# Performance work log

Hardware: AMD Instinct MI355X
Metric: run time of the kernel (lower is better)

The kernel has to match this reference:

```python
import jax, jax.numpy as jnp
import numpy as np

B, S, D, H, R, P = 4, 8192, 512, 8, 64, 4
HD = D // H  # 64
EPS = 1e-6


def _sketch_p4(z, G1, G2):
    # sketchwithnegativity(z, 2): M1 = M2 = z
    inv_sqrt_r = 1.0 / np.sqrt(R).astype(np.float32)
    half = inv_sqrt_r * ((z @ G1) * (z @ G2))  # [B,H,S,R]
    return half * half  # sketch(): half * half for p=4


def setup_inputs() -> dict:
    key = jax.random.key(0)
    ks = jax.random.split(key, 16)
    lin = lambda k: jax.random.normal(k, (D, D), jnp.float32) * (1.0 / np.sqrt(D))
    g = lambda k: jax.random.normal(k, (HD, R), jnp.float32) * (1.0 / np.sqrt(R))
    return {
        "x": jax.random.normal(ks[0], (B, S, D), jnp.float32),
        "Wq": lin(ks[1]), "bq": jnp.zeros((D,), jnp.float32),
        "Wk": lin(ks[2]), "bk": jnp.zeros((D,), jnp.float32),
        "Wv": lin(ks[3]), "bv": jnp.zeros((D,), jnp.float32),
        "Wp": lin(ks[4]), "bp": jnp.zeros((D,), jnp.float32),
        "gamma_q": jnp.ones((1,), jnp.float32), "beta_q": jnp.zeros((1,), jnp.float32),
        "gamma_k": jnp.ones((1,), jnp.float32), "beta_k": jnp.zeros((1,), jnp.float32),
        "qG1": g(ks[5]), "qG2": g(ks[6]),
        "kG1": g(ks[7]), "kG2": g(ks[8]),
    }


def reference(x, Wq, bq, Wk, bk, Wv, bv, Wp, bp,
              gamma_q, beta_q, gamma_k, beta_k, qG1, qG2, kG1, kG2):
    b, s, d = x.shape
    split = lambda t: t.reshape(b, s, H, HD).transpose(0, 2, 1, 3)  # [B,H,S,HD]
    q = split(x @ Wq + bq)
    k = split(x @ Wk + bk)
    v = split(x @ Wv + bv)
    q = gamma_q * q + beta_q
    k = gamma_k * k + beta_k
    phi_q = _sketch_p4(q, qG1, qG2)  # [B,H,S,R]
    phi_k = _sketch_p4(k, kG1, kG2)  # [B,H,S,R]
    # linear-attention form of attn = (phi_q phi_k^T) / rowsum; avoids [S,S]
    kv = jnp.einsum('bhsr,bhsd->bhrd', phi_k, v)          # [B,H,R,HD]
    ksum = phi_k.sum(axis=2)                              # [B,H,R]
    num = jnp.einsum('bhqr,bhrd->bhqd', phi_q, kv)        # [B,H,S,HD]
    den = jnp.einsum('bhqr,bhr->bhq', phi_q, ksum) + EPS  # [B,H,S]
    out = num / den[..., None]
    out = out.transpose(0, 2, 1, 3).reshape(b, s, d)
    return out @ Wp + bp
```

## Files before the change

### kernel.cpp

```cpp
#include <hip/hip_runtime.h>
#include <hip/hip_bf16.h>


#define SEQ 8192

typedef __attribute__((ext_vector_type(8))) short bf16x8;
typedef __attribute__((ext_vector_type(4))) float f32x4;

__device__ __forceinline__ unsigned short f2b(float f) {
    union { float f; unsigned int i; } v; v.f = f;
    unsigned int r = v.i + 0x7fffu + ((v.i >> 16) & 1u);
    return (unsigned short)(r >> 16);
}
__device__ __forceinline__ float b2f(unsigned short u) {
    union { unsigned int i; float f; } v; v.i = ((unsigned int)u) << 16; return v.f;
}

#if __has_builtin(__builtin_amdgcn_global_load_lds)
#define ASYNC_CP 1
#endif

__device__ __forceinline__ void cp16(const unsigned short* g, unsigned short* l) {
#ifdef ASYNC_CP
    __builtin_amdgcn_global_load_lds(
        (const __attribute__((address_space(1))) unsigned int*)g,
        (__attribute__((address_space(3))) unsigned int*)l, 16, 0, 0);
#endif
}

__global__ __launch_bounds__(256) void convert_x(
    const float* __restrict__ x, unsigned short* __restrict__ xb)
{
    size_t i = ((size_t)blockIdx.x * 256 + threadIdx.x) * 8;
    float4 a = *(const float4*)&x[i];
    float4 b = *(const float4*)&x[i + 4];
    ushort4 o1 = { f2b(a.x), f2b(a.y), f2b(a.z), f2b(a.w) };
    ushort4 o2 = { f2b(b.x), f2b(b.y), f2b(b.z), f2b(b.w) };
    *(ushort4*)&xb[i]     = o1;
    *(ushort4*)&xb[i + 4] = o2;
}

__global__ __launch_bounds__(256) void convert_wT(
    const float* __restrict__ Wv, const float* __restrict__ Wp,
    unsigned short* __restrict__ WTf, unsigned short* __restrict__ WTp)
{
    const int z = blockIdx.z;
    const float* W = (z == 0) ? Wv : Wp;
    unsigned short* O = (z == 0) ? (WTf + (size_t)2048 * 512) : WTp;
    __shared__ float t[32][33];
    const int tid = threadIdx.x;
    const int tx = tid & 31, ty = tid >> 5;
    const int k0 = blockIdx.x * 32, n0 = blockIdx.y * 32;
    #pragma unroll
    for (int i = 0; i < 4; ++i)
        t[ty + 8 * i][tx] = W[(size_t)(k0 + ty + 8 * i) * 512 + n0 + tx];
    __syncthreads();
    #pragma unroll
    for (int i = 0; i < 4; ++i)
        O[(size_t)(n0 + ty + 8 * i) * 512 + k0 + tx] = f2b(t[tx][ty + 8 * i]);
}

__global__ __launch_bounds__(256) void precompute_wc(
    const float* __restrict__ Wq, const float* __restrict__ bq,
    const float* __restrict__ Wk, const float* __restrict__ bk,
    const float* __restrict__ bv,
    const float* __restrict__ gq, const float* __restrict__ bbq,
    const float* __restrict__ gk, const float* __restrict__ bbk,
    const float* __restrict__ qG1, const float* __restrict__ qG2,
    const float* __restrict__ kG1, const float* __restrict__ kG2,
    unsigned short* __restrict__ WTf, float* __restrict__ cvec)
{
    const int bi = blockIdx.x;
    const int tid = threadIdx.x;
    if (bi == 32) {
        if (blockIdx.y == 0)
            for (int i = tid; i < 512; i += 256) cvec[2048 + i] = bv[i];
        return;
    }
    const int zz = bi >> 4, h = (bi >> 1) & 7, p = bi & 1;
    const float* W    = zz ? Wk : Wq;
    const float* bias = zz ? bk : bq;
    const float* G    = zz ? (p ? kG2 : kG1) : (p ? qG2 : qG1);
    const float  gamma = zz ? gk[0] : gq[0];
    const float  beta  = zz ? bbk[0] : bbq[0];

    __shared__ float Gs[64][65];
    for (int i = tid; i < 4096; i += 256) Gs[i >> 6][i & 63] = G[i];
    __syncthreads();

    const int rr = tid & 63, kg = tid >> 6;
    const int jc = zz * 1024 + h * 128 + rr * 2 + p;
    const int k0 = blockIdx.y * 32;
    for (int k = k0 + kg; k < k0 + 32; k += 4) {
        float s = 0.f;
        const float* wrow = &W[(size_t)k * 512 + h * 64];
        #pragma unroll 8
        for (int j = 0; j < 64; ++j) s = fmaf(wrow[j], Gs[j][rr], s);
        WTf[(size_t)jc * 512 + k] = f2b(gamma * s);
    }
    if (kg == 0 && blockIdx.y == 0) {
        float cb = 0.f, cg = 0.f;
        #pragma unroll 8
        for (int j = 0; j < 64; ++j) {
            cb = fmaf(bias[h * 64 + j], Gs[j][rr], cb);
            cg += Gs[j][rr];
        }
        cvec[jc] = gamma * cb + beta * cg;
    }
}

__global__ __launch_bounds__(256) void gemm_mfma_fused(
    const unsigned short* __restrict__ xb,
    const unsigned short* __restrict__ WTf,
    const float* __restrict__ cvec,
    unsigned short* __restrict__ PHIQ, unsigned short* __restrict__ PHIK,
    unsigned short* __restrict__ Vb)
{
    __shared__ __align__(16) unsigned short As[128 * 32];
    __shared__ __align__(16) unsigned short Bs[128 * 32];

    const int tid = threadIdx.x;
    const int w = tid >> 6, lane = tid & 63;
    const int n0 = blockIdx.x * 128;
    const int j0 = blockIdx.y * 128;
    const int wr = w >> 1, wc = w & 1;

    const int r0 = w * 32 + (lane >> 2);
    const int kq = (lane & 3) * 8;
    const unsigned short* gA = &xb[(size_t)(n0 + r0) * 512 + kq];
    const unsigned short* gB = &WTf[(size_t)(j0 + r0) * 512 + kq];
    unsigned short* lA = &As[(w * 32) * 32];
    unsigned short* lB = &Bs[(w * 32) * 32];

    f32x4 acc[4][4];
    #pragma unroll
    for (int i = 0; i < 4; ++i)
        #pragma unroll
        for (int j = 0; j < 4; ++j) { acc[i][j] = (f32x4){0.f, 0.f, 0.f, 0.f}; }

    for (int k0 = 0; k0 < 512; k0 += 32) {
        __syncthreads();
#ifdef ASYNC_CP
        cp16(gA + k0, lA);
        cp16(gA + 16 * 512 + k0, lA + 16 * 32);
        cp16(gB + k0, lB);
        cp16(gB + 16 * 512 + k0, lB + 16 * 32);
#else
        { uint4 v = *(const uint4*)(gA + k0);            *(uint4*)(lA + (size_t)lane * 8) = v; }
        { uint4 v = *(const uint4*)(gA + 16 * 512 + k0); *(uint4*)(lA + 16 * 32 + (size_t)lane * 8) = v; }
        { uint4 v = *(const uint4*)(gB + k0);            *(uint4*)(lB + (size_t)lane * 8) = v; }
        { uint4 v = *(const uint4*)(gB + 16 * 512 + k0); *(uint4*)(lB + 16 * 32 + (size_t)lane * 8) = v; }
#endif
        __syncthreads();

        bf16x8 af[4], bfr[4];
        #pragma unroll
        for (int i = 0; i < 4; ++i) {
            af[i]  = *(const bf16x8*)&As[(wr * 64 + i * 16 + (lane & 15)) * 32 + (lane >> 4) * 8];
            bfr[i] = *(const bf16x8*)&Bs[(wc * 64 + i * 16 + (lane & 15)) * 32 + (lane >> 4) * 8];
        }
        #pragma unroll
        for (int mi = 0; mi < 4; ++mi)
            #pragma unroll
            for (int ni = 0; ni < 4; ++ni)
                acc[mi][ni] = __builtin_amdgcn_mfma_f32_16x16x32_bf16(
                    af[mi], bfr[ni], acc[mi][ni], 0, 0, 0);
    }

    #pragma unroll
    for (int ni = 0; ni < 4; ++ni) {
        const int jcol = j0 + wc * 64 + ni * 16 + (lane & 15);
        const float cv = cvec[jcol];
        if (jcol < 2048) {
            const int zq = jcol >> 10;
            const int lc = jcol & 1023;
            const int h = lc >> 7, rr = (lc >> 1) & 63;
            unsigned short* dst = zq ? PHIK : PHIQ;
            #pragma unroll
            for (int mi = 0; mi < 4; ++mi) {
                #pragma unroll
                for (int r = 0; r < 4; ++r) {
                    float u = acc[mi][ni][r] + cv;
                    float up = __shfl_xor(u, 1);
                    float hh = 0.125f * u * up;
                    float phi = hh * hh;
                    if ((lane & 1) == 0) {
                        const int t = n0 + wr * 64 + mi * 16 + (lane >> 4) * 4 + r;
                        const int b = t >> 13, s = t & (SEQ - 1);
                        dst[((size_t)(b * 8 + h) * SEQ + s) * 64 + rr] = f2b(phi);
                    }
                }
            }
        } else {
            const int n = jcol - 2048;
            const int h = n >> 6, hd = n & 63;
            #pragma unroll
            for (int mi = 0; mi < 4; ++mi) {
                #pragma unroll
                for (int r = 0; r < 4; ++r) {
                    const int t = n0 + wr * 64 + mi * 16 + (lane >> 4) * 4 + r;
                    const int b = t >> 13, s = t & (SEQ - 1);
                    Vb[((size_t)(b * 8 + h) * SEQ + s) * 64 + hd] =
                        f2b(acc[mi][ni][r] + cv);
                }
            }
        }
    }
}

__global__ __launch_bounds__(256) void gemm_mfma_final(
    const unsigned short* __restrict__ Ab,
    const unsigned short* __restrict__ WTp,
    const float* __restrict__ bias, float* __restrict__ out)
{
    __shared__ __align__(16) unsigned short As[128 * 32];
    __shared__ __align__(16) unsigned short Bs[128 * 32];

    const int tid = threadIdx.x;
    const int w = tid >> 6, lane = tid & 63;
    const int n0 = blockIdx.x * 128;
    const int j0 = blockIdx.y * 128;
    const int wr = w >> 1, wc = w & 1;

    const int r0 = w * 32 + (lane >> 2);
    const int kq = (lane & 3) * 8;
    const unsigned short* gA = &Ab[(size_t)(n0 + r0) * 512 + kq];
    const unsigned short* gB = &WTp[(size_t)(j0 + r0) * 512 + kq];
    unsigned short* lA = &As[(w * 32) * 32];
    unsigned short* lB = &Bs[(w * 32) * 32];

    f32x4 acc[4][4];
    #pragma unroll
    for (int i = 0; i < 4; ++i)
        #pragma unroll
        for (int j = 0; j < 4; ++j) { acc[i][j] = (f32x4){0.f, 0.f, 0.f, 0.f}; }

    for (int k0 = 0; k0 < 512; k0 += 32) {
        __syncthreads();
#ifdef ASYNC_CP
        cp16(gA + k0, lA);
        cp16(gA + 16 * 512 + k0, lA + 16 * 32);
        cp16(gB + k0, lB);
        cp16(gB + 16 * 512 + k0, lB + 16 * 32);
#else
        { uint4 v = *(const uint4*)(gA + k0);            *(uint4*)(lA + (size_t)lane * 8) = v; }
        { uint4 v = *(const uint4*)(gA + 16 * 512 + k0); *(uint4*)(lA + 16 * 32 + (size_t)lane * 8) = v; }
        { uint4 v = *(const uint4*)(gB + k0);            *(uint4*)(lB + (size_t)lane * 8) = v; }
        { uint4 v = *(const uint4*)(gB + 16 * 512 + k0); *(uint4*)(lB + 16 * 32 + (size_t)lane * 8) = v; }
#endif
        __syncthreads();

        bf16x8 af[4], bfr[4];
        #pragma unroll
        for (int i = 0; i < 4; ++i) {
            af[i]  = *(const bf16x8*)&As[(wr * 64 + i * 16 + (lane & 15)) * 32 + (lane >> 4) * 8];
            bfr[i] = *(const bf16x8*)&Bs[(wc * 64 + i * 16 + (lane & 15)) * 32 + (lane >> 4) * 8];
        }
        #pragma unroll
        for (int mi = 0; mi < 4; ++mi)
            #pragma unroll
            for (int ni = 0; ni < 4; ++ni)
                acc[mi][ni] = __builtin_amdgcn_mfma_f32_16x16x32_bf16(
                    af[mi], bfr[ni], acc[mi][ni], 0, 0, 0);
    }

    #pragma unroll
    for (int ni = 0; ni < 4; ++ni) {
        const int jcol = j0 + wc * 64 + ni * 16 + (lane & 15);
        const float bvv = bias[jcol];
        #pragma unroll
        for (int mi = 0; mi < 4; ++mi) {
            #pragma unroll
            for (int r = 0; r < 4; ++r) {
                const int t = n0 + wr * 64 + mi * 16 + (lane >> 4) * 4 + r;
                out[(size_t)t * 512 + jcol] = acc[mi][ni][r] + bvv;
            }
        }
    }
}

__global__ __launch_bounds__(256) void kv_partial(
    const unsigned short* __restrict__ PHIK, const unsigned short* __restrict__ Vb,
    float* __restrict__ KVP, float* __restrict__ KSP)
{
    const int bh = blockIdx.x, ch = blockIdx.y;
    const unsigned short* phik = PHIK + ((size_t)bh * SEQ + ch * 256) * 64;
    const unsigned short* v    = Vb   + ((size_t)bh * SEQ + ch * 256) * 64;
    __shared__ float ps[64][68];
    __shared__ float vs[64][68];
    const int tid = threadIdx.x;
    const int tx = tid & 15, ty = tid >> 4;
    const int r0 = ty * 4, c0 = tx * 4;
    float acc[4][4] = {};
    float ks[4] = {};
    for (int sub = 0; sub < 4; ++sub) {
        __syncthreads();
        {
            const int r = tid >> 4, c4 = (tid & 15) * 4;
            #pragma unroll
            for (int it = 0; it < 4; ++it) {
                ushort4 p = *(const ushort4*)&phik[(size_t)(sub * 64 + r + 16 * it) * 64 + c4];
                ushort4 vv = *(const ushort4*)&v[(size_t)(sub * 64 + r + 16 * it) * 64 + c4];
                ps[r + 16 * it][c4 + 0] = b2f(p.x);  ps[r + 16 * it][c4 + 1] = b2f(p.y);
                ps[r + 16 * it][c4 + 2] = b2f(p.z);  ps[r + 16 * it][c4 + 3] = b2f(p.w);
                vs[r + 16 * it][c4 + 0] = b2f(vv.x); vs[r + 16 * it][c4 + 1] = b2f(vv.y);
                vs[r + 16 * it][c4 + 2] = b2f(vv.z); vs[r + 16 * it][c4 + 3] = b2f(vv.w);
            }
        }
        __syncthreads();
        #pragma unroll 4
        for (int s = 0; s < 64; ++s) {
            float4 p4 = *(const float4*)&ps[s][r0];
            float4 v4 = *(const float4*)&vs[s][c0];
            float pa[4] = { p4.x, p4.y, p4.z, p4.w };
            float va[4] = { v4.x, v4.y, v4.z, v4.w };
            #pragma unroll
            for (int a = 0; a < 4; ++a) {
                ks[a] += pa[a];
                #pragma unroll
                for (int bb = 0; bb < 4; ++bb)
                    acc[a][bb] = fmaf(pa[a], va[bb], acc[a][bb]);
            }
        }
    }
    #pragma unroll
    for (int a = 0; a < 4; ++a) {
        float4 o = { acc[a][0], acc[a][1], acc[a][2], acc[a][3] };
        *(float4*)&KVP[((size_t)(bh * 32 + ch) * 64 + r0 + a) * 64 + c0] = o;
    }
    if (tx == 0) {
        #pragma unroll
        for (int a = 0; a < 4; ++a)
            KSP[(bh * 32 + ch) * 64 + r0 + a] = ks[a];
    }
}

__global__ __launch_bounds__(256) void kv_reduce(
    const float* __restrict__ KVP, const float* __restrict__ KSP,
    float* __restrict__ KV, float* __restrict__ KS)
{
    const int bh = blockIdx.x, tid = threadIdx.x;
    for (int e = tid; e < 4096; e += 256) {
        float s = 0.f;
        for (int c = 0; c < 32; ++c) s += KVP[(size_t)(bh * 32 + c) * 4096 + e];
        KV[(size_t)bh * 4096 + e] = s;
    }
    if (tid < 64) {
        float s = 0.f;
        for (int c = 0; c < 32; ++c) s += KSP[(bh * 32 + c) * 64 + tid];
        KS[bh * 64 + tid] = s;
    }
}

__global__ __launch_bounds__(256) void attn_out(
    const unsigned short* __restrict__ PHIQ, const float* __restrict__ KV,
    const float* __restrict__ KS, unsigned short* __restrict__ OAb)
{
    const int bh = blockIdx.x;
    const int b = bh >> 3, h = bh & 7;
    __shared__ float kvs[64][68];
    __shared__ float pqs[64][65];
    __shared__ float kss[64];
    const int tid = threadIdx.x;
    const int tx = tid & 15, ty = tid >> 4;
    const int s0 = blockIdx.y * 64;
    {
        const int r = tid >> 4, c4 = (tid & 15) * 4;
        #pragma unroll
        for (int it = 0; it < 4; ++it) {
            float4 kvv = *(const float4*)&KV[(size_t)bh * 4096 + (size_t)(r + 16 * it) * 64 + c4];
            ushort4 pq = *(const ushort4*)&PHIQ[((size_t)bh * SEQ + s0 + r + 16 * it) * 64 + c4];
            *(float4*)&kvs[r + 16 * it][c4] = kvv;
            pqs[r + 16 * it][c4 + 0] = b2f(pq.x); pqs[r + 16 * it][c4 + 1] = b2f(pq.y);
            pqs[r + 16 * it][c4 + 2] = b2f(pq.z); pqs[r + 16 * it][c4 + 3] = b2f(pq.w);
        }
        if (tid < 64) kss[tid] = KS[bh * 64 + tid];
    }
    __syncthreads();
    const int r0 = ty * 4, c0 = tx * 4;
    float num[4][4] = {};
    float den[4] = { 1e-6f, 1e-6f, 1e-6f, 1e-6f };
    #pragma unroll 4
    for (int i = 0; i < 64; ++i) {
        float pr[4] = { pqs[r0][i], pqs[r0 + 1][i], pqs[r0 + 2][i], pqs[r0 + 3][i] };
        float4 kv4 = *(const float4*)&kvs[i][c0];
        float kva[4] = { kv4.x, kv4.y, kv4.z, kv4.w };
        float ksv = kss[i];
        #pragma unroll
        for (int a = 0; a < 4; ++a) {
            den[a] = fmaf(pr[a], ksv, den[a]);
            #pragma unroll
            for (int bb = 0; bb < 4; ++bb)
                num[a][bb] = fmaf(pr[a], kva[bb], num[a][bb]);
        }
    }
    #pragma unroll
    for (int a = 0; a < 4; ++a) {
        const float inv = 1.0f / den[a];
        ushort4 o = { f2b(num[a][0] * inv), f2b(num[a][1] * inv),
                      f2b(num[a][2] * inv), f2b(num[a][3] * inv) };
        const int s = s0 + r0 + a;
        *(ushort4*)&OAb[((size_t)(b * SEQ + s)) * 512 + h * 64 + c0] = o;
    }
}

extern "C" void kernel_launch(void* const* d_in, const int* in_sizes, int n_in,
                              void* d_out, int out_size, void* d_ws, size_t ws_size,
                              hipStream_t stream)
{
    (void)in_sizes; (void)n_in; (void)out_size; (void)ws_size;
    const float* x   = (const float*)d_in[0];
    const float* Wq  = (const float*)d_in[1];
    const float* bq  = (const float*)d_in[2];
    const float* Wk  = (const float*)d_in[3];
    const float* bk  = (const float*)d_in[4];
    const float* Wv  = (const float*)d_in[5];
    const float* bv  = (const float*)d_in[6];
    const float* Wp  = (const float*)d_in[7];
    const float* bp  = (const float*)d_in[8];
    const float* gq  = (const float*)d_in[9];
    const float* bbq = (const float*)d_in[10];
    const float* gk  = (const float*)d_in[11];
    const float* bbk = (const float*)d_in[12];
    const float* qG1 = (const float*)d_in[13];
    const float* qG2 = (const float*)d_in[14];
    const float* kG1 = (const float*)d_in[15];
    const float* kG2 = (const float*)d_in[16];

    unsigned short* PHIQ = (unsigned short*)d_ws;
    unsigned short* PHIK = PHIQ + 16777216;
    unsigned short* Vb   = PHIK + 16777216;
    unsigned short* xb   = Vb   + 16777216;
    unsigned short* OAb  = xb   + 16777216;
    unsigned short* WTf  = OAb  + 16777216;
    unsigned short* WTp  = WTf  + 2560 * 512;
    float* cvec = (float*)(WTp + 262144);
    float* KVP  = cvec + 2560;
    float* KSP  = KVP + 4194304;
    float* KV   = KSP + 65536;
    float* KS   = KV + 131072;
    float* out  = (float*)d_out;

    hipLaunchKernelGGL(convert_x, dim3(8192), dim3(256), 0, stream, x, xb);
    hipLaunchKernelGGL(convert_wT, dim3(16, 16, 2), dim3(256), 0, stream,
                       Wv, Wp, WTf, WTp);
    hipLaunchKernelGGL(precompute_wc, dim3(33, 16), dim3(256), 0, stream,
                       Wq, bq, Wk, bk, bv, gq, bbq, gk, bbk,
                       qG1, qG2, kG1, kG2, WTf, cvec);
    hipLaunchKernelGGL(gemm_mfma_fused, dim3(256, 20), dim3(256), 0, stream,
                       xb, WTf, cvec, PHIQ, PHIK, Vb);
    hipLaunchKernelGGL(kv_partial, dim3(32, 32), dim3(256), 0, stream,
                       PHIK, Vb, KVP, KSP);
    hipLaunchKernelGGL(kv_reduce, dim3(32), dim3(256), 0, stream, KVP, KSP, KV, KS);
    hipLaunchKernelGGL(attn_out, dim3(32, 128), dim3(256), 0, stream,
                       PHIQ, KV, KS, OAb);
    hipLaunchKernelGGL(gemm_mfma_final, dim3(256, 4), dim3(256), 0, stream,
                       OAb, WTp, bp, out);
}
```

Baseline: 403.8 us.

## Move KV and attention to MFMA, transpose PHIK/V, stage epilogues through LDS

The fused projection GEMM now writes phi_k and V transposed (feature-major) through an LDS staging buffer so global stores are 16-byte coalesced. Both GEMMs also XOR-swizzle their LDS tile columns to cut bank conflicts. kv_partial and attn_out move from scalar FMA loops to MFMA bf16 kernels: ksum comes from an MFMA against a ones vector, and KV/ksum are split into hi+lo bf16 parts to keep precision. kv_reduce is spread over more blocks. The changes add LDS use and extra syncs in the GEMM epilogue, and the bf16 split may carry some rounding risk.

```diff
diff --git a/kernel.cpp b/kernel.cpp
--- a/kernel.cpp
+++ b/kernel.cpp
@@ -113,11 +113,12 @@
     const unsigned short* __restrict__ xb,
     const unsigned short* __restrict__ WTf,
     const float* __restrict__ cvec,
-    unsigned short* __restrict__ PHIQ, unsigned short* __restrict__ PHIK,
-    unsigned short* __restrict__ Vb)
+    unsigned short* __restrict__ PHIQ, unsigned short* __restrict__ PHIKT,
+    unsigned short* __restrict__ VT)
 {
     __shared__ __align__(16) unsigned short As[128 * 32];
     __shared__ __align__(16) unsigned short Bs[128 * 32];
+    __shared__ __align__(16) unsigned short ep[9216];
 
     const int tid = threadIdx.x;
     const int w = tid >> 6, lane = tid & 63;
@@ -126,7 +127,7 @@
     const int wr = w >> 1, wc = w & 1;
 
     const int r0 = w * 32 + (lane >> 2);
-    const int kq = (lane & 3) * 8;
+    const int kq = (((lane & 3) ^ ((lane >> 2) & 3)) * 8);
     const unsigned short* gA = &xb[(size_t)(n0 + r0) * 512 + kq];
     const unsigned short* gB = &WTf[(size_t)(j0 + r0) * 512 + kq];
     unsigned short* lA = &As[(w * 32) * 32];
@@ -137,6 +138,8 @@
     for (int i = 0; i < 4; ++i)
         #pragma unroll
         for (int j = 0; j < 4; ++j) { acc[i][j] = (f32x4){0.f, 0.f, 0.f, 0.f}; }
+
+    const int cr = (((lane >> 4) ^ (lane & 3)) * 8);
 
     for (int k0 = 0; k0 < 512; k0 += 32) {
         __syncthreads();
@@ -156,8 +159,8 @@
         bf16x8 af[4], bfr[4];
         #pragma unroll
         for (int i = 0; i < 4; ++i) {
-            af[i]  = *(const bf16x8*)&As[(wr * 64 + i * 16 + (lane & 15)) * 32 + (lane >> 4) * 8];
-            bfr[i] = *(const bf16x8*)&Bs[(wc * 64 + i * 16 + (lane & 15)) * 32 + (lane >> 4) * 8];
+            af[i]  = *(const bf16x8*)&As[(wr * 64 + i * 16 + (lane & 15)) * 32 + cr];
+            bfr[i] = *(const bf16x8*)&Bs[(wc * 64 + i * 16 + (lane & 15)) * 32 + cr];
         }
         #pragma unroll
         for (int mi = 0; mi < 4; ++mi)
@@ -167,43 +170,83 @@
                     af[mi], bfr[ni], acc[mi][ni], 0, 0, 0);
     }
 
-    #pragma unroll
-    for (int ni = 0; ni < 4; ++ni) {
-        const int jcol = j0 + wc * 64 + ni * 16 + (lane & 15);
-        const float cv = cvec[jcol];
-        if (jcol < 2048) {
-            const int zq = jcol >> 10;
-            const int lc = jcol & 1023;
-            const int h = lc >> 7, rr = (lc >> 1) & 63;
-            unsigned short* dst = zq ? PHIK : PHIQ;
+    const int bq = n0 >> 13;
+    const int sq = n0 & (SEQ - 1);
+
+    if (j0 < 1024) {
+        const int h = j0 >> 7;
+        #pragma unroll
+        for (int ni = 0; ni < 4; ++ni) {
+            const int loc = wc * 64 + ni * 16 + (lane & 15);
+            const float cv = cvec[j0 + loc];
+            const int rr = loc >> 1;
             #pragma unroll
-            for (int mi = 0; mi < 4; ++mi) {
+            for (int mi = 0; mi < 4; ++mi)
                 #pragma unroll
                 for (int r = 0; r < 4; ++r) {
                     float u = acc[mi][ni][r] + cv;
                     float up = __shfl_xor(u, 1);
                     float hh = 0.125f * u * up;
                     float phi = hh * hh;
-                    if ((lane & 1) == 0) {
-                        const int t = n0 + wr * 64 + mi * 16 + (lane >> 4) * 4 + r;
-                        const int b = t >> 13, s = t & (SEQ - 1);
-                        dst[((size_t)(b * 8 + h) * SEQ + s) * 64 + rr] = f2b(phi);
-                    }
+                    if ((lane & 1) == 0)
+                        ep[(wr * 64 + mi * 16 + (lane >> 4) * 4 + r) * 72 + rr] = f2b(phi);
+                }
+        }
+        __syncthreads();
+        for (int i = tid; i < 1024; i += 256) {
+            const int tok = i >> 3, ch = i & 7;
+            *(uint4*)&PHIQ[((size_t)(bq * 8 + h) * SEQ + sq + tok) * 64 + ch * 8] =
+                *(const uint4*)&ep[tok * 72 + ch * 8];
+        }
+    } else if (j0 < 2048) {
+        const int h = (j0 >> 7) & 7;
+        #pragma unroll
+        for (int ni = 0; ni < 4; ++ni) {
+            const int loc = wc * 64 + ni * 16 + (lane & 15);
+            const float cv = cvec[j0 + loc];
+            const int rr = loc >> 1;
+            #pragma unroll
+            for (int mi = 0; mi < 4; ++mi)
+                #pragma unroll
+                for (int r = 0; r < 4; ++r) {
+                    float u = acc[mi][ni][r] + cv;
+                    float up = __shfl_xor(u, 1);
+                    float hh = 0.125f * u * up;
+                    float phi = hh * hh;
+                    if ((lane & 1) == 0)
+                        ep[rr * 136 + wr * 64 + mi * 16 + (lane >> 4) * 4 + r] = f2b(phi);
+                }
+        }
+        __syncthreads();
+        for (int i = tid; i < 1024; i += 256) {
+            const int row = i >> 4, ch = i & 15;
+            *(uint4*)&PHIKT[((size_t)((bq * 8 + h) * 64 + row)) * SEQ + sq + ch * 8] =
+                *(const uint4*)&ep[row * 136 + ch * 8];
+        }
+    } else {
+        #pragma unroll
+        for (int half = 0; half < 2; ++half) {
+            if (wc == half) {
+                #pragma unroll
+                for (int ni = 0; ni < 4; ++ni) {
+                    const int loc = ni * 16 + (lane & 15);
+                    const float cv = cvec[j0 + half * 64 + loc];
+                    #pragma unroll
+                    for (int mi = 0; mi < 4; ++mi)
+                        #pragma unroll
+                        for (int r = 0; r < 4; ++r)
+                            ep[loc * 136 + wr * 64 + mi * 16 + (lane >> 4) * 4 + r] =
+                                f2b(acc[mi][ni][r] + cv);
                 }
             }
-        } else {
-            const int n = jcol - 2048;
-            const int h = n >> 6, hd = n & 63;
-            #pragma unroll
-            for (int mi = 0; mi < 4; ++mi) {
-                #pragma unroll
-                for (int r = 0; r < 4; ++r) {
-                    const int t = n0 + wr * 64 + mi * 16 + (lane >> 4) * 4 + r;
-                    const int b = t >> 13, s = t & (SEQ - 1);
-                    Vb[((size_t)(b * 8 + h) * SEQ + s) * 64 + hd] =
-                        f2b(acc[mi][ni][r] + cv);
-                }
+            __syncthreads();
+            for (int i = tid; i < 1024; i += 256) {
+                const int row = i >> 4, ch = i & 15;
+                const int n = (j0 - 2048) + half * 64 + row;
+                *(uint4*)&VT[((size_t)(bq * 512 + n)) * SEQ + sq + ch * 8] =
+                    *(const uint4*)&ep[row * 136 + ch * 8];
             }
+            __syncthreads();
         }
     }
 }
@@ -223,7 +266,7 @@
     const int wr = w >> 1, wc = w & 1;
 
     const int r0 = w * 32 + (lane >> 2);
-    const int kq = (lane & 3) * 8;
+    const int kq = (((lane & 3) ^ ((lane >> 2) & 3)) * 8);
     const unsigned short* gA = &Ab[(size_t)(n0 + r0) * 512 + kq];
     const unsigned short* gB = &WTp[(size_t)(j0 + r0) * 512 + kq];
     unsigned short* lA = &As[(w * 32) * 32];
@@ -234,6 +277,8 @@
     for (int i = 0; i < 4; ++i)
         #pragma unroll
         for (int j = 0; j < 4; ++j) { acc[i][j] = (f32x4){0.f, 0.f, 0.f, 0.f}; }
+
+    const int cr = (((lane >> 4) ^ (lane & 3)) * 8);
 
     for (int k0 = 0; k0 < 512; k0 += 32) {
         __syncthreads();
@@ -253,8 +298,8 @@
         bf16x8 af[4], bfr[4];
         #pragma unroll
         for (int i = 0; i < 4; ++i) {
-            af[i]  = *(const bf16x8*)&As[(wr * 64 + i * 16 + (lane & 15)) * 32 + (lane >> 4) * 8];
-            bfr[i] = *(const bf16x8*)&Bs[(wc * 64 + i * 16 + (lane & 15)) * 32 + (lane >> 4) * 8];
+            af[i]  = *(const bf16x8*)&As[(wr * 64 + i * 16 + (lane & 15)) * 32 + cr];
+            bfr[i] = *(const bf16x8*)&Bs[(wc * 64 + i * 16 + (lane & 15)) * 32 + cr];
         }
         #pragma unroll
         for (int mi = 0; mi < 4; ++mi)
@@ -279,59 +324,47 @@
     }
 }
 
-__global__ __launch_bounds__(256) void kv_partial(
-    const unsigned short* __restrict__ PHIK, const unsigned short* __restrict__ Vb,
+__global__ __launch_bounds__(256) void kv_mfma(
+    const unsigned short* __restrict__ PHIKT, const unsigned short* __restrict__ VT,
     float* __restrict__ KVP, float* __restrict__ KSP)
 {
-    const int bh = blockIdx.x, ch = blockIdx.y;
-    const unsigned short* phik = PHIK + ((size_t)bh * SEQ + ch * 256) * 64;
-    const unsigned short* v    = Vb   + ((size_t)bh * SEQ + ch * 256) * 64;
-    __shared__ float ps[64][68];
-    __shared__ float vs[64][68];
+    const int bh = blockIdx.x, seg = blockIdx.y;
     const int tid = threadIdx.x;
-    const int tx = tid & 15, ty = tid >> 4;
-    const int r0 = ty * 4, c0 = tx * 4;
-    float acc[4][4] = {};
-    float ks[4] = {};
-    for (int sub = 0; sub < 4; ++sub) {
-        __syncthreads();
-        {
-            const int r = tid >> 4, c4 = (tid & 15) * 4;
-            #pragma unroll
-            for (int it = 0; it < 4; ++it) {
-                ushort4 p = *(const ushort4*)&phik[(size_t)(sub * 64 + r + 16 * it) * 64 + c4];
-                ushort4 vv = *(const ushort4*)&v[(size_t)(sub * 64 + r + 16 * it) * 64 + c4];
-                ps[r + 16 * it][c4 + 0] = b2f(p.x);  ps[r + 16 * it][c4 + 1] = b2f(p.y);
-                ps[r + 16 * it][c4 + 2] = b2f(p.z);  ps[r + 16 * it][c4 + 3] = b2f(p.w);
-                vs[r + 16 * it][c4 + 0] = b2f(vv.x); vs[r + 16 * it][c4 + 1] = b2f(vv.y);
-                vs[r + 16 * it][c4 + 2] = b2f(vv.z); vs[r + 16 * it][c4 + 3] = b2f(vv.w);
-            }
-        }
-        __syncthreads();
-        #pragma unroll 4
-        for (int s = 0; s < 64; ++s) {
-            float4 p4 = *(const float4*)&ps[s][r0];
-            float4 v4 = *(const float4*)&vs[s][c0];
-            float pa[4] = { p4.x, p4.y, p4.z, p4.w };
-            float va[4] = { v4.x, v4.y, v4.z, v4.w };
-            #pragma unroll
-            for (int a = 0; a < 4; ++a) {
-                ks[a] += pa[a];
-                #pragma unroll
-                for (int bb = 0; bb < 4; ++bb)
-                    acc[a][bb] = fmaf(pa[a], va[bb], acc[a][bb]);
-            }
-        }
-    }
-    #pragma unroll
-    for (int a = 0; a < 4; ++a) {
-        float4 o = { acc[a][0], acc[a][1], acc[a][2], acc[a][3] };
-        *(float4*)&KVP[((size_t)(bh * 32 + ch) * 64 + r0 + a) * 64 + c0] = o;
-    }
-    if (tx == 0) {
-        #pragma unroll
-        for (int a = 0; a < 4; ++a)
-            KSP[(bh * 32 + ch) * 64 + r0 + a] = ks[a];
+    const int w = tid >> 6, lane = tid & 63;
+    const size_t pbase =
+        ((size_t)bh * 64 + w * 16 + (lane & 15)) * SEQ + seg * 256 + (lane >> 4) * 8;
+    const size_t vbase =
+        ((size_t)((bh >> 3) * 512 + (bh & 7) * 64 + (lane & 15))) * SEQ
+        + seg * 256 + (lane >> 4) * 8;
+
+    f32x4 acc[4], ks;
+    #pragma unroll
+    for (int nt = 0; nt < 4; ++nt) acc[nt] = (f32x4){0.f, 0.f, 0.f, 0.f};
+    ks = (f32x4){0.f, 0.f, 0.f, 0.f};
+    bf16x8 ones;
+    #pragma unroll
+    for (int i = 0; i < 8; ++i) ones[i] = (short)0x3f80;
+
+    #pragma unroll 2
+    for (int k = 0; k < 256; k += 32) {
+        bf16x8 a = *(const bf16x8*)&PHIKT[pbase + k];
+        ks = __builtin_amdgcn_mfma_f32_16x16x32_bf16(a, ones, ks, 0, 0, 0);
+        #pragma unroll
+        for (int nt = 0; nt < 4; ++nt) {
+            bf16x8 bb = *(const bf16x8*)&VT[vbase + (size_t)nt * 16 * SEQ + k];
+            acc[nt] = __builtin_amdgcn_mfma_f32_16x16x32_bf16(a, bb, acc[nt], 0, 0, 0);
+        }
+    }
+
+    float* kvp = &KVP[((size_t)bh * 32 + seg) * 4096];
+    #pragma unroll
+    for (int nt = 0; nt < 4; ++nt) {
+        float4 o = { acc[nt][0], acc[nt][1], acc[nt][2], acc[nt][3] };
+        *(float4*)&kvp[(nt * 16 + (lane & 15)) * 64 + w * 16 + (lane >> 4) * 4] = o;
+    }
+    if ((lane & 15) == 0) {
+        float4 o = { ks[0], ks[1], ks[2], ks[3] };
+        *(float4*)&KSP[((size_t)bh * 32 + seg) * 64 + w * 16 + (lane >> 4) * 4] = o;
     }
 }
 
@@ -339,68 +372,78 @@
     const float* __restrict__ KVP, const float* __restrict__ KSP,
     float* __restrict__ KV, float* __restrict__ KS)
 {
-    const int bh = blockIdx.x, tid = threadIdx.x;
-    for (int e = tid; e < 4096; e += 256) {
+    const int bh = blockIdx.x;
+    const int e0 = blockIdx.y * 512;
+    for (int e = e0 + threadIdx.x; e < e0 + 512; e += 256) {
         float s = 0.f;
+        #pragma unroll 8
         for (int c = 0; c < 32; ++c) s += KVP[(size_t)(bh * 32 + c) * 4096 + e];
         KV[(size_t)bh * 4096 + e] = s;
     }
-    if (tid < 64) {
+    if (blockIdx.y == 0 && threadIdx.x < 64) {
         float s = 0.f;
-        for (int c = 0; c < 32; ++c) s += KSP[(bh * 32 + c) * 64 + tid];
-        KS[bh * 64 + tid] = s;
-    }
-}
-
-__global__ __launch_bounds__(256) void attn_out(
+        for (int c = 0; c < 32; ++c) s += KSP[(bh * 32 + c) * 64 + threadIdx.x];
+        KS[bh * 64 + threadIdx.x] = s;
+    }
+}
+
+__global__ __launch_bounds__(256) void attn_mfma(
     const unsigned short* __restrict__ PHIQ, const float* __restrict__ KV,
     const float* __restrict__ KS, unsigned short* __restrict__ OAb)
 {
-    const int bh = blockIdx.x;
+    __shared__ __align__(16) unsigned short bpad[144 * 72];
+    const int bh = blockIdx.x, st = blockIdx.y;
+    const int tid = threadIdx.x;
     const int b = bh >> 3, h = bh & 7;
-    __shared__ float kvs[64][68];
-    __shared__ float pqs[64][65];
-    __shared__ float kss[64];
-    const int tid = threadIdx.x;
-    const int tx = tid & 15, ty = tid >> 4;
-    const int s0 = blockIdx.y * 64;
-    {
-        const int r = tid >> 4, c4 = (tid & 15) * 4;
-        #pragma unroll
-        for (int it = 0; it < 4; ++it) {
-            float4 kvv = *(const float4*)&KV[(size_t)bh * 4096 + (size_t)(r + 16 * it) * 64 + c4];
-            ushort4 pq = *(const ushort4*)&PHIQ[((size_t)bh * SEQ + s0 + r + 16 * it) * 64 + c4];
-            *(float4*)&kvs[r + 16 * it][c4] = kvv;
-            pqs[r + 16 * it][c4 + 0] = b2f(pq.x); pqs[r + 16 * it][c4 + 1] = b2f(pq.y);
-            pqs[r + 16 * it][c4 + 2] = b2f(pq.z); pqs[r + 16 * it][c4 + 3] = b2f(pq.w);
-        }
-        if (tid < 64) kss[tid] = KS[bh * 64 + tid];
+
+    for (int i = tid; i < 144 * 64; i += 256) {
+        const int n = i >> 6, r = i & 63;
+        float val;
+        if (n < 64)        val = KV[(size_t)bh * 4096 + n * 64 + r];
+        else if (n < 128)  { float x = KV[(size_t)bh * 4096 + (n - 64) * 64 + r];
+                             val = x - b2f(f2b(x)); }
+        else if (n == 128) val = KS[bh * 64 + r];
+        else if (n == 129) { float x = KS[bh * 64 + r]; val = x - b2f(f2b(x)); }
+        else               val = 0.f;
+        bpad[n * 72 + r] = f2b(val);
     }
     __syncthreads();
-    const int r0 = ty * 4, c0 = tx * 4;
-    float num[4][4] = {};
-    float den[4] = { 1e-6f, 1e-6f, 1e-6f, 1e-6f };
-    #pragma unroll 4
-    for (int i = 0; i < 64; ++i) {
-        float pr[4] = { pqs[r0][i], pqs[r0 + 1][i], pqs[r0 + 2][i], pqs[r0 + 3][i] };
-        float4 kv4 = *(const float4*)&kvs[i][c0];
-        float kva[4] = { kv4.x, kv4.y, kv4.z, kv4.w };
-        float ksv = kss[i];
-        #pragma unroll
-        for (int a = 0; a < 4; ++a) {
-            den[a] = fmaf(pr[a], ksv, den[a]);
+
+    const int w = tid >> 6, lane = tid & 63;
+    bf16x8 bf[9][2];
+    #pragma unroll
+    for (int nt = 0; nt < 9; ++nt) {
+        const unsigned short* bp = &bpad[(nt * 16 + (lane & 15)) * 72 + (lane >> 4) * 8];
+        bf[nt][0] = *(const bf16x8*)bp;
+        bf[nt][1] = *(const bf16x8*)(bp + 32);
+    }
+
+    const int tw = st * 256 + w * 64;
+    #pragma unroll
+    for (int mt = 0; mt < 4; ++mt) {
+        const unsigned short* ap =
+            &PHIQ[((size_t)bh * SEQ + tw + mt * 16 + (lane & 15)) * 64 + (lane >> 4) * 8];
+        bf16x8 a0 = *(const bf16x8*)ap;
+        bf16x8 a1 = *(const bf16x8*)(ap + 32);
+        f32x4 acc[9];
+        #pragma unroll
+        for (int nt = 0; nt < 9; ++nt) acc[nt] = (f32x4){0.f, 0.f, 0.f, 0.f};
+        #pragma unroll
+        for (int nt = 0; nt < 9; ++nt) {
+            acc[nt] = __builtin_amdgcn_mfma_f32_16x16x32_bf16(a0, bf[nt][0], acc[nt], 0, 0, 0);
+            acc[nt] = __builtin_amdgcn_mfma_f32_16x16x32_bf16(a1, bf[nt][1], acc[nt], 0, 0, 0);
+        }
+        #pragma unroll
+        for (int r4 = 0; r4 < 4; ++r4) {
+            const float den = __shfl(acc[8][r4], (lane & 48)) +
+                              __shfl(acc[8][r4], (lane & 48) + 1) + 1e-6f;
+            const float inv = 1.0f / den;
+            const int s = tw + mt * 16 + (lane >> 4) * 4 + r4;
             #pragma unroll
-            for (int bb = 0; bb < 4; ++bb)
-                num[a][bb] = fmaf(pr[a], kva[bb], num[a][bb]);
-        }
-    }
-    #pragma unroll
-    for (int a = 0; a < 4; ++a) {
-        const float inv = 1.0f / den[a];
-        ushort4 o = { f2b(num[a][0] * inv), f2b(num[a][1] * inv),
-                      f2b(num[a][2] * inv), f2b(num[a][3] * inv) };
-        const int s = s0 + r0 + a;
-        *(ushort4*)&OAb[((size_t)(b * SEQ + s)) * 512 + h * 64 + c0] = o;
+            for (int nt = 0; nt < 4; ++nt)
+                OAb[((size_t)b * SEQ + s) * 512 + h * 64 + nt * 16 + (lane & 15)] =
+                    f2b((acc[nt][r4] + acc[nt + 4][r4]) * inv);
+        }
     }
 }
 
@@ -427,13 +470,13 @@
     const float* kG1 = (const float*)d_in[15];
     const float* kG2 = (const float*)d_in[16];
 
-    unsigned short* PHIQ = (unsigned short*)d_ws;
-    unsigned short* PHIK = PHIQ + 16777216;
-    unsigned short* Vb   = PHIK + 16777216;
-    unsigned short* xb   = Vb   + 16777216;
-    unsigned short* OAb  = xb   + 16777216;
-    unsigned short* WTf  = OAb  + 16777216;
-    unsigned short* WTp  = WTf  + 2560 * 512;
+    unsigned short* PHIQ  = (unsigned short*)d_ws;
+    unsigned short* PHIKT = PHIQ + 16777216;
+    unsigned short* VT    = PHIKT + 16777216;
+    unsigned short* xb    = VT   + 16777216;
+    unsigned short* OAb   = xb   + 16777216;
+    unsigned short* WTf   = OAb  + 16777216;
+    unsigned short* WTp   = WTf  + 2560 * 512;
     float* cvec = (float*)(WTp + 262144);
     float* KVP  = cvec + 2560;
     float* KSP  = KVP + 4194304;
@@ -448,11 +491,11 @@
                        Wq, bq, Wk, bk, bv, gq, bbq, gk, bbk,
                        qG1, qG2, kG1, kG2, WTf, cvec);
     hipLaunchKernelGGL(gemm_mfma_fused, dim3(256, 20), dim3(256), 0, stream,
-                       xb, WTf, cvec, PHIQ, PHIK, Vb);
-    hipLaunchKernelGGL(kv_partial, dim3(32, 32), dim3(256), 0, stream,
-                       PHIK, Vb, KVP, KSP);
-    hipLaunchKernelGGL(kv_reduce, dim3(32), dim3(256), 0, stream, KVP, KSP, KV, KS);
-    hipLaunchKernelGGL(attn_out, dim3(32, 128), dim3(256), 0, stream,
+                       xb, WTf, cvec, PHIQ, PHIKT, VT);
+    hipLaunchKernelGGL(kv_mfma, dim3(32, 32), dim3(256), 0, stream,
+                       PHIKT, VT, KVP, KSP);
+    hipLaunchKernelGGL(kv_reduce, dim3(32, 8), dim3(256), 0, stream, KVP, KSP, KV, KS);
+    hipLaunchKernelGGL(attn_mfma, dim3(32, 32), dim3(256), 0, stream,
                        PHIQ, KV, KS, OAb);
     hipLaunchKernelGGL(gemm_mfma_final, dim3(256, 4), dim3(256), 0, stream,
                        OAb, WTp, bp, out);
```

New measurement: 417.0 us. +3.3%, slower.
